# Performance work log

Hardware: AMD Instinct MI355X
Metric: run time of the kernel (lower is better)

Reference implementation:

```python
import jax, jax.numpy as jnp
import numpy as np

B, V = 256, 128000

def setup_inputs() -> dict:
    key = jax.random.key(0)
    k1, k2 = jax.random.split(key)
    logits = jax.random.normal(k1, (B, V), dtype=jnp.float32)
    # temperatures in [0.5, 1.5) to avoid degenerate near-zero temps
    temperatures = jax.random.uniform(k2, (B,), dtype=jnp.float32, minval=0.5, maxval=1.5)
    return {"logits": logits, "temperatures": temperatures, "top_k": 50}

def reference(logits, temperatures, top_k):
    # temperature scale (logits.float().div_(temps[:, None]))
    scaled = logits.astype(jnp.float32) / temperatures[:, None]          # [B, V]
    # top-k threshold: k-th largest value per row
    kth = jax.lax.top_k(scaled, top_k)[0][:, -1:]                        # [B, 1]
    # mask everything strictly below the k-th value to -inf
    masked = jnp.where(scaled < kth, -jnp.inf, scaled)                   # [B, V]
    # softmax + multinomial(1)  ==  categorical over masked logits
    samples = jax.random.categorical(jax.random.key(42), masked, axis=-1)  # [B]
    return samples
```

## Files before the change

### kernel.cpp

```cpp
#include <hip/hip_runtime.h>

#define THREADS 1024
#define BINS 4096
#define NCOPY 4
#define CAP 4096

__device__ __forceinline__ unsigned rotl32(unsigned x, unsigned r) {
  return (x << r) | (x >> (32u - r));
}

__device__ __forceinline__ unsigned threefry_xor_0_42(unsigned x0, unsigned x1) {
  const unsigned k0 = 0u, k1 = 42u, k2 = 0u ^ 42u ^ 0x1BD11BDAu;
  x0 += k0; x1 += k1;
#define TF_R(r) { x0 += x1; x1 = rotl32(x1, r); x1 ^= x0; }
  TF_R(13) TF_R(15) TF_R(26) TF_R(6)
  x0 += k1; x1 += k2 + 1u;
  TF_R(17) TF_R(29) TF_R(16) TF_R(24)
  x0 += k2; x1 += k0 + 2u;
  TF_R(13) TF_R(15) TF_R(26) TF_R(6)
  x0 += k0; x1 += k1 + 3u;
  TF_R(17) TF_R(29) TF_R(16) TF_R(24)
  x0 += k1; x1 += k2 + 4u;
  TF_R(13) TF_R(15) TF_R(26) TF_R(6)
  x0 += k2; x1 += k0 + 5u;
#undef TF_R
  return x0 ^ x1;
}

__device__ __forceinline__ float gumbel_at(unsigned flat) {
  unsigned bits = threefry_xor_0_42(0u, flat);
  float fl = __uint_as_float((bits >> 9) | 0x3F800000u) - 1.0f;
  const float tiny = 1.17549435e-38f;
  float u = fmaxf(fl + tiny, tiny);
  return -logf(-logf(u));
}

__device__ __forceinline__ unsigned f2k(float f) {
  unsigned b = __float_as_uint(f);
  return (b & 0x80000000u) ? ~b : (b ^ 0x80000000u);
}
__device__ __forceinline__ float k2f(unsigned k) {
  unsigned b = (k & 0x80000000u) ? (k ^ 0x80000000u) : ~k;
  return __uint_as_float(b);
}

__global__ __launch_bounds__(THREADS) void sampler_kernel(
    const float* __restrict__ logits, const float* __restrict__ temps,
    const int* __restrict__ topk_ptr, int* __restrict__ out, int V) {
  const int row = blockIdx.x;
  const int tid = threadIdx.x;
  const unsigned K = (unsigned)(*topk_ptr);

  const float* rowp = logits + (size_t)row * (size_t)V;
  const float4* rowp4 = (const float4*)rowp;
  const int nv4 = V >> 2;

  __shared__ unsigned hist[NCOPY][BINS];
  __shared__ unsigned cand_key[CAP];
  __shared__ unsigned cand_idx[CAP];
  __shared__ float    rv[THREADS];
  __shared__ unsigned ri[THREADS];
  __shared__ unsigned ncand, sBstar, sAbove, sK50;

  for (int i = tid; i < NCOPY * BINS; i += THREADS) ((unsigned*)hist)[i] = 0u;
  if (tid == 0) { ncand = 0u; sBstar = 0u; sAbove = 0u; sK50 = 0u; }
  __syncthreads();

  {
    unsigned* myh = hist[(tid >> 6) & (NCOPY - 1)];
    for (int i = tid; i < nv4; i += THREADS) {
      float4 v = rowp4[i];
      atomicAdd(&myh[f2k(v.x) >> 20], 1u);
      atomicAdd(&myh[f2k(v.y) >> 20], 1u);
      atomicAdd(&myh[f2k(v.z) >> 20], 1u);
      atomicAdd(&myh[f2k(v.w) >> 20], 1u);
    }
  }
  __syncthreads();

  for (int i = tid; i < BINS; i += THREADS) {
    unsigned s = hist[0][i];
#pragma unroll
    for (int cpy = 1; cpy < NCOPY; ++cpy) s += hist[cpy][i];
    hist[0][i] = s;
  }
  __syncthreads();

  if (tid < 64) {
    const int lane = tid;
    unsigned s = 0;
    for (int k = 0; k < 64; ++k) s += hist[0][lane * 64 + k];
    unsigned suf = s;
#pragma unroll
    for (int off = 1; off < 64; off <<= 1) {
      unsigned o = __shfl_down(suf, off);
      if (lane + off < 64) suf += o;
    }
    unsigned sufn = __shfl_down(suf, 1);
    if (lane == 63) sufn = 0u;
    if (suf >= K && sufn < K) {
      unsigned run = sufn;
      for (int k = 63; k >= 0; --k) {
        unsigned h = hist[0][lane * 64 + k];
        unsigned nr = run + h;
        if (run < K && nr >= K) { sBstar = (unsigned)(lane * 64 + k); sAbove = run; }
        run = nr;
      }
    }
  }
  __syncthreads();

  const unsigned Bstar = sBstar;
  const unsigned cntAbove = sAbove;
  const unsigned long long binCeilP1 = ((unsigned long long)(Bstar + 1u)) << 20;
  const unsigned lowKey = (Bstar >= 1u) ? ((Bstar - 1u) << 20) : 0u;
  const float t = temps[row];
  const unsigned rowBase = (unsigned)row * (unsigned)V;

  float bestV = -INFINITY;
  unsigned bestI = 0xFFFFFFFFu;

  for (int i = tid; i < nv4; i += THREADS) {
    float4 v = rowp4[i];
    float f[4] = {v.x, v.y, v.z, v.w};
#pragma unroll
    for (int e = 0; e < 4; ++e) {
      unsigned key = f2k(f[e]);
      if (key < lowKey) continue;
      unsigned col = (unsigned)(i * 4 + e);
      if ((unsigned long long)key >= binCeilP1) {
        float sj = f[e] / t;
        float val = sj + gumbel_at(rowBase + col);
        if (val > bestV || (val == bestV && col < bestI)) { bestV = val; bestI = col; }
      } else {
        unsigned p = atomicAdd(&ncand, 1u);
        if (p < CAP) { cand_key[p] = key; cand_idx[p] = col; }
      }
    }
  }
  __syncthreads();

  const unsigned c = min(ncand, (unsigned)CAP);
  for (unsigned i = tid; i < c; i += THREADS) {
    unsigned ki = cand_key[i];
    unsigned gt = 0, eq = 0;
    for (unsigned j = 0; j < c; ++j) {
      unsigned kj = cand_key[j];
      gt += (kj > ki) ? 1u : 0u;
      eq += (kj == ki) ? 1u : 0u;
    }
    if (cntAbove + gt < K && cntAbove + gt + eq >= K) sK50 = ki;
  }
  __syncthreads();

  const float l50 = k2f(sK50);
  const float s50 = l50 / t;
  for (unsigned i = tid; i < c; i += THREADS) {
    unsigned col = cand_idx[i];
    if (col >= (unsigned)V) continue;
    float sj = k2f(cand_key[i]) / t;
    if (sj >= s50) {
      float val = sj + gumbel_at(rowBase + col);
      if (val > bestV || (val == bestV && col < bestI)) { bestV = val; bestI = col; }
    }
  }

  rv[tid] = bestV; ri[tid] = bestI;
  __syncthreads();
  for (int off = THREADS / 2; off > 0; off >>= 1) {
    if (tid < off) {
      float v2 = rv[tid + off]; unsigned i2 = ri[tid + off];
      if (v2 > rv[tid] || (v2 == rv[tid] && i2 < ri[tid])) { rv[tid] = v2; ri[tid] = i2; }
    }
    __syncthreads();
  }
  if (tid == 0) out[row] = (int)((ri[0] < (unsigned)V) ? ri[0] : 0u);
}

extern "C" void kernel_launch(void* const* d_in, const int* in_sizes, int n_in,
                              void* d_out, int out_size, void* d_ws, size_t ws_size,
                              hipStream_t stream) {
  const float* logits = (const float*)d_in[0];
  const float* temps  = (const float*)d_in[1];
  const int*   topk   = (const int*)d_in[2];
  int* out = (int*)d_out;

  const int B = in_sizes[1];
  const int V = in_sizes[0] / B;

  sampler_kernel<<<B, THREADS, 0, stream>>>(logits, temps, topk, out, V);
}
```

Baseline: 214.6 us.

## Add speculative fixed-threshold candidate filter with histogram fallback for top-k sampling

Before anything else, a single pass collects only logits whose raw value is at or above a fixed floor (2.5) into the shared candidate buffer. The k-th largest value is then found exactly among those candidates by rank counting. When the count fits the buffer, is at least K, and the threshold sits safely above the floor, the kernel skips the full-row histogram pass and the second filtering pass, which would roughly halve global reads and remove most shared-memory atomics. Otherwise it falls back to the original histogram path, now using a single histogram copy and a scalar tail loop. The speed-up depends on the logit distribution putting only a modest number of values above the floor; rows that miss it pay an extra read pass.

```diff
diff --git a/kernel.cpp b/kernel.cpp
--- a/kernel.cpp
+++ b/kernel.cpp
@@ -2,8 +2,9 @@
 
 #define THREADS 1024
 #define BINS 4096
-#define NCOPY 4
 #define CAP 4096
+#define FLOOR_KEY 0xC0200000u
+#define MARGIN 8u
 
 __device__ __forceinline__ unsigned rotl32(unsigned x, unsigned r) {
   return (x << r) | (x >> (32u - r));
@@ -54,107 +55,156 @@
   const float* rowp = logits + (size_t)row * (size_t)V;
   const float4* rowp4 = (const float4*)rowp;
   const int nv4 = V >> 2;
-
-  __shared__ unsigned hist[NCOPY][BINS];
+  const int half4 = nv4 >> 1;
+
+  __shared__ unsigned hist[BINS];
   __shared__ unsigned cand_key[CAP];
   __shared__ unsigned cand_idx[CAP];
   __shared__ float    rv[THREADS];
   __shared__ unsigned ri[THREADS];
   __shared__ unsigned ncand, sBstar, sAbove, sK50;
 
-  for (int i = tid; i < NCOPY * BINS; i += THREADS) ((unsigned*)hist)[i] = 0u;
   if (tid == 0) { ncand = 0u; sBstar = 0u; sAbove = 0u; sK50 = 0u; }
   __syncthreads();
 
-  {
-    unsigned* myh = hist[(tid >> 6) & (NCOPY - 1)];
+  for (int i = tid; i < half4; i += THREADS) {
+    float4 a = rowp4[i];
+    float4 b = rowp4[i + half4];
+    float f[8] = {a.x, a.y, a.z, a.w, b.x, b.y, b.z, b.w};
+#pragma unroll
+    for (int e = 0; e < 8; ++e) {
+      unsigned key = f2k(f[e]);
+      if (key >= FLOOR_KEY) {
+        unsigned col = (unsigned)((e < 4 ? i : i + half4) * 4 + (e & 3));
+        unsigned p = atomicAdd(&ncand, 1u);
+        if (p < CAP) { cand_key[p] = key; cand_idx[p] = col; }
+      }
+    }
+  }
+  for (int j = (half4 * 2) * 4 + tid; j < V; j += THREADS) {
+    unsigned key = f2k(rowp[j]);
+    if (key >= FLOOR_KEY) {
+      unsigned p = atomicAdd(&ncand, 1u);
+      if (p < CAP) { cand_key[p] = key; cand_idx[p] = (unsigned)j; }
+    }
+  }
+  __syncthreads();
+
+  const bool tryFast = (ncand >= K && ncand <= (unsigned)CAP);
+  unsigned c = min(ncand, (unsigned)CAP);
+
+  if (tryFast) {
+    for (unsigned i = tid; i < c; i += THREADS) {
+      unsigned ki = cand_key[i];
+      unsigned gt = 0, eq = 0;
+      for (unsigned j = 0; j < c; ++j) {
+        unsigned kj = cand_key[j];
+        gt += (kj > ki) ? 1u : 0u;
+        eq += (kj == ki) ? 1u : 0u;
+      }
+      if (gt < K && gt + eq >= K) sK50 = ki;
+    }
+  }
+  __syncthreads();
+
+  const bool fastOK = tryFast && (sK50 >= FLOOR_KEY + MARGIN);
+
+  float bestV = -INFINITY;
+  unsigned bestI = 0xFFFFFFFFu;
+  const float t = temps[row];
+  const unsigned rowBase = (unsigned)row * (unsigned)V;
+
+  if (!fastOK) {
+    for (int i = tid; i < BINS; i += THREADS) hist[i] = 0u;
+    if (tid == 0) ncand = 0u;
+    __syncthreads();
+
     for (int i = tid; i < nv4; i += THREADS) {
       float4 v = rowp4[i];
-      atomicAdd(&myh[f2k(v.x) >> 20], 1u);
-      atomicAdd(&myh[f2k(v.y) >> 20], 1u);
-      atomicAdd(&myh[f2k(v.z) >> 20], 1u);
-      atomicAdd(&myh[f2k(v.w) >> 20], 1u);
-    }
-  }
-  __syncthreads();
-
-  for (int i = tid; i < BINS; i += THREADS) {
-    unsigned s = hist[0][i];
+      atomicAdd(&hist[f2k(v.x) >> 20], 1u);
+      atomicAdd(&hist[f2k(v.y) >> 20], 1u);
+      atomicAdd(&hist[f2k(v.z) >> 20], 1u);
+      atomicAdd(&hist[f2k(v.w) >> 20], 1u);
+    }
+    for (int j = nv4 * 4 + tid; j < V; j += THREADS) atomicAdd(&hist[f2k(rowp[j]) >> 20], 1u);
+    __syncthreads();
+
+    if (tid < 64) {
+      const int lane = tid;
+      unsigned s = 0;
+      for (int k = 0; k < 64; ++k) s += hist[lane * 64 + k];
+      unsigned suf = s;
 #pragma unroll
-    for (int cpy = 1; cpy < NCOPY; ++cpy) s += hist[cpy][i];
-    hist[0][i] = s;
-  }
-  __syncthreads();
-
-  if (tid < 64) {
-    const int lane = tid;
-    unsigned s = 0;
-    for (int k = 0; k < 64; ++k) s += hist[0][lane * 64 + k];
-    unsigned suf = s;
+      for (int off = 1; off < 64; off <<= 1) {
+        unsigned o = __shfl_down(suf, off);
+        if (lane + off < 64) suf += o;
+      }
+      unsigned sufn = __shfl_down(suf, 1);
+      if (lane == 63) sufn = 0u;
+      if (suf >= K && sufn < K) {
+        unsigned run = sufn;
+        for (int k = 63; k >= 0; --k) {
+          unsigned h = hist[lane * 64 + k];
+          unsigned nr = run + h;
+          if (run < K && nr >= K) { sBstar = (unsigned)(lane * 64 + k); sAbove = run; }
+          run = nr;
+        }
+      }
+    }
+    __syncthreads();
+
+    const unsigned Bstar = sBstar;
+    const unsigned cntAbove = sAbove;
+    const unsigned long long binCeilP1 = ((unsigned long long)(Bstar + 1u)) << 20;
+    const unsigned lowKey = (Bstar >= 1u) ? ((Bstar - 1u) << 20) : 0u;
+
+    for (int i = tid; i < nv4; i += THREADS) {
+      float4 v = rowp4[i];
+      float f[4] = {v.x, v.y, v.z, v.w};
 #pragma unroll
-    for (int off = 1; off < 64; off <<= 1) {
-      unsigned o = __shfl_down(suf, off);
-      if (lane + off < 64) suf += o;
-    }
-    unsigned sufn = __shfl_down(suf, 1);
-    if (lane == 63) sufn = 0u;
-    if (suf >= K && sufn < K) {
-      unsigned run = sufn;
-      for (int k = 63; k >= 0; --k) {
-        unsigned h = hist[0][lane * 64 + k];
-        unsigned nr = run + h;
-        if (run < K && nr >= K) { sBstar = (unsigned)(lane * 64 + k); sAbove = run; }
-        run = nr;
-      }
-    }
-  }
-  __syncthreads();
-
-  const unsigned Bstar = sBstar;
-  const unsigned cntAbove = sAbove;
-  const unsigned long long binCeilP1 = ((unsigned long long)(Bstar + 1u)) << 20;
-  const unsigned lowKey = (Bstar >= 1u) ? ((Bstar - 1u) << 20) : 0u;
-  const float t = temps[row];
-  const unsigned rowBase = (unsigned)row * (unsigned)V;
-
-  float bestV = -INFINITY;
-  unsigned bestI = 0xFFFFFFFFu;
-
-  for (int i = tid; i < nv4; i += THREADS) {
-    float4 v = rowp4[i];
-    float f[4] = {v.x, v.y, v.z, v.w};
-#pragma unroll
-    for (int e = 0; e < 4; ++e) {
-      unsigned key = f2k(f[e]);
+      for (int e = 0; e < 4; ++e) {
+        unsigned key = f2k(f[e]);
+        if (key < lowKey) continue;
+        unsigned col = (unsigned)(i * 4 + e);
+        if ((unsigned long long)key >= binCeilP1) {
+          float sj = f[e] / t;
+          float val = sj + gumbel_at(rowBase + col);
+          if (val > bestV || (val == bestV && col < bestI)) { bestV = val; bestI = col; }
+        } else {
+          unsigned p = atomicAdd(&ncand, 1u);
+          if (p < CAP) { cand_key[p] = key; cand_idx[p] = col; }
+        }
+      }
+    }
+    for (int j = nv4 * 4 + tid; j < V; j += THREADS) {
+      unsigned key = f2k(rowp[j]);
       if (key < lowKey) continue;
-      unsigned col = (unsigned)(i * 4 + e);
       if ((unsigned long long)key >= binCeilP1) {
-        float sj = f[e] / t;
-        float val = sj + gumbel_at(rowBase + col);
-        if (val > bestV || (val == bestV && col < bestI)) { bestV = val; bestI = col; }
+        float sj = rowp[j] / t;
+        float val = sj + gumbel_at(rowBase + (unsigned)j);
+        if (val > bestV || (val == bestV && (unsigned)j < bestI)) { bestV = val; bestI = (unsigned)j; }
       } else {
         unsigned p = atomicAdd(&ncand, 1u);
-        if (p < CAP) { cand_key[p] = key; cand_idx[p] = col; }
-      }
-    }
-  }
-  __syncthreads();
-
-  const unsigned c = min(ncand, (unsigned)CAP);
-  for (unsigned i = tid; i < c; i += THREADS) {
-    unsigned ki = cand_key[i];
-    unsigned gt = 0, eq = 0;
-    for (unsigned j = 0; j < c; ++j) {
-      unsigned kj = cand_key[j];
-      gt += (kj > ki) ? 1u : 0u;
-      eq += (kj == ki) ? 1u : 0u;
-    }
-    if (cntAbove + gt < K && cntAbove + gt + eq >= K) sK50 = ki;
-  }
-  __syncthreads();
-
-  const float l50 = k2f(sK50);
-  const float s50 = l50 / t;
+        if (p < CAP) { cand_key[p] = key; cand_idx[p] = (unsigned)j; }
+      }
+    }
+    __syncthreads();
+
+    c = min(ncand, (unsigned)CAP);
+    for (unsigned i = tid; i < c; i += THREADS) {
+      unsigned ki = cand_key[i];
+      unsigned gt = 0, eq = 0;
+      for (unsigned j = 0; j < c; ++j) {
+        unsigned kj = cand_key[j];
+        gt += (kj > ki) ? 1u : 0u;
+        eq += (kj == ki) ? 1u : 0u;
+      }
+      if (cntAbove + gt < K && cntAbove + gt + eq >= K) sK50 = ki;
+    }
+    __syncthreads();
+  }
+
+  const float s50 = k2f(sK50) / t;
   for (unsigned i = tid; i < c; i += THREADS) {
     unsigned col = cand_idx[i];
     if (col >= (unsigned)V) continue;
```

After: 219.5 us. 1.02x slower.
